# Kernel optimization log

Hardware: AMD Instinct MI355X
Metric: run time of the kernel (lower is better)

Reference implementation:

```python
import jax, jax.numpy as jnp
import numpy as np

HEADS = 4
DIM_HEAD = 64
DIM = 256
FMAP = 64
SCALE = DIM_HEAD ** -0.5


def setup_inputs() -> dict:
    key = jax.random.key(0)
    k1, k2, k3, k4 = jax.random.split(key, 4)
    inner = HEADS * DIM_HEAD
    fmap = jax.random.normal(k1, (4, DIM, FMAP, FMAP), dtype=jnp.float32)
    # 1x1 conv weight for qkv projection: (3*inner_dim, dim)
    w_qkv = jax.random.normal(k2, (3 * inner, DIM), dtype=jnp.float32) * (DIM ** -0.5)
    # AbsPosEmb parameters, initialized as randn * dim_head**-0.5 (as in BoTNet)
    pos_height = jax.random.normal(k3, (FMAP, DIM_HEAD), dtype=jnp.float32) * SCALE
    pos_width = jax.random.normal(k4, (FMAP, DIM_HEAD), dtype=jnp.float32) * SCALE
    return {"fmap": fmap, "w_qkv": w_qkv, "pos_height": pos_height, "pos_width": pos_width}


def reference(fmap, w_qkv, pos_height, pos_width):
    b, c, h, w = fmap.shape
    hw = h * w
    # 1x1 conv (no bias) == channel matmul
    qkv = jnp.einsum('bchw,oc->bohw', fmap, w_qkv)  # (b, 3*inner, h, w)
    q, k, v = jnp.split(qkv, 3, axis=1)
    # replicate torch .view(b, heads, h*w, -1): raw row-major reshape
    q = q.reshape(b, HEADS, hw, DIM_HEAD) * SCALE
    k = k.reshape(b, HEADS, hw, DIM_HEAD)
    v = v.reshape(b, HEADS, hw, DIM_HEAD)
    sim = jnp.einsum('bhid,bhjd->bhij', q, k)  # (b, heads, hw, hw)
    # absolute positional bias: emb[j] = height[y] + width[x], j = y*w + x
    emb = (pos_height[:, None, :] + pos_width[None, :, :]).reshape(hw, DIM_HEAD)
    sim = sim + jnp.einsum('bhid,jd->bhij', q, emb)
    attn = jax.nn.softmax(sim, axis=-1)
    out = jnp.einsum('bhij,bhjd->bhid', attn, v)  # (b, heads, hw, dim_head)
    # replicate torch .view(b, heads*dim_head, h, w): raw reshape
    return out.reshape(b, HEADS * DIM_HEAD, h, w)
```

## Files before the change

### kernel.cpp

```cpp
#include <hip/hip_runtime.h>


typedef float  f32x4  __attribute__((ext_vector_type(4)));
typedef __bf16 bf16x8 __attribute__((ext_vector_type(8)));
typedef __bf16 bf16x4 __attribute__((ext_vector_type(4)));

__device__ inline float fast_exp2(float x) {
#if __has_builtin(__builtin_amdgcn_exp2f)
  return __builtin_amdgcn_exp2f(x);
#else
  return exp2f(x);
#endif
}

__global__ __launch_bounds__(256) void qkv_proj(
    const float* __restrict__ fmap, const float* __restrict__ w,
    const float* __restrict__ ph,   const float* __restrict__ pw,
    __bf16* __restrict__ Qw, __bf16* __restrict__ Kw, __bf16* __restrict__ Vw)
{
  constexpr int LS = 136;
  __shared__ __bf16 As[64 * LS];
  __shared__ __bf16 Bs[64 * LS];
  const int tid  = threadIdx.x;
  const int wv   = tid >> 6;
  const int lane = tid & 63;
  const int quad = lane >> 4, l15 = lane & 15;
  const int n0 = blockIdx.x * 64;
  const int m0 = blockIdx.y * 64;
  const int b  = blockIdx.z;

  f32x4 sacc[4] = {};

  for (int ks = 0; ks < 2; ++ks) {
    const int kbase = ks * 128;
#pragma unroll
    for (int i = 0; i < 8; ++i) {
      int id = tid + i * 256;
      int r  = id >> 5;
      int c4 = (id & 31) * 4;
      f32x4 v = *(const f32x4*)(w + (size_t)(m0 + r) * 256 + kbase + c4);
      bf16x4 o; o[0]=(__bf16)v[0]; o[1]=(__bf16)v[1]; o[2]=(__bf16)v[2]; o[3]=(__bf16)v[3];
      *(bf16x4*)(&As[r * LS + c4]) = o;
    }
#pragma unroll
    for (int i = 0; i < 2; ++i) {
      int id = tid + i * 256;
      int sg = id & 15;
      int kg = id >> 4;
      const float* base = fmap + ((size_t)b * 256 + kbase + 4 * kg) * 4096 + n0 + 4 * sg;
      f32x4 v0 = *(const f32x4*)(base);
      f32x4 v1 = *(const f32x4*)(base + 4096);
      f32x4 v2 = *(const f32x4*)(base + 8192);
      f32x4 v3 = *(const f32x4*)(base + 12288);
#pragma unroll
      for (int j = 0; j < 4; ++j) {
        bf16x4 o; o[0]=(__bf16)v0[j]; o[1]=(__bf16)v1[j]; o[2]=(__bf16)v2[j]; o[3]=(__bf16)v3[j];
        *(bf16x4*)(&Bs[(4 * sg + j) * LS + 4 * kg]) = o;
      }
    }
    __syncthreads();
#pragma unroll
    for (int k0 = 0; k0 < 128; k0 += 32) {
      bf16x8 af = *(const bf16x8*)(&As[(16 * wv + l15) * LS + k0 + 8 * quad]);
#pragma unroll
      for (int t = 0; t < 4; ++t) {
        bf16x8 bt = *(const bf16x8*)(&Bs[(16 * t + l15) * LS + k0 + 8 * quad]);
        sacc[t] = __builtin_amdgcn_mfma_f32_16x16x32_bf16(af, bt, sacc[t], 0, 0, 0);
      }
    }
    __syncthreads();
  }

  const int region = blockIdx.y >> 2;
  const int obase  = (blockIdx.y & 3) * 64;
#pragma unroll
  for (int t = 0; t < 4; ++t) {
#pragma unroll
    for (int rr = 0; rr < 4; ++rr) {
      int row = 16 * wv + 4 * quad + rr;
      int s   = n0 + 16 * t + l15;
      float val = sacc[t][rr];
      size_t off = ((size_t)(b * 256 + obase + row)) * 4096 + s;
      if (region == 0) {
        Qw[off] = (__bf16)(val * 0.18033688f);
      } else if (region == 1) {
        float bias = ph[row * 64 + (s & 63)] + pw[(s >> 6) * 64 + (s & 63)];
        Kw[off] = (__bf16)(val + bias);
      } else {
        Vw[off] = (__bf16)val;
      }
    }
  }
}

__global__ __launch_bounds__(256) void v_transpose(
    const __bf16* __restrict__ Vw, __bf16* __restrict__ Vt)
{
  __shared__ __bf16 T[64 * 72];
  const int tid = threadIdx.x;
  const int j0  = blockIdx.x * 64;
  const int bh  = blockIdx.y;
  const __bf16* src = Vw + (size_t)bh * 262144;
#pragma unroll
  for (int i = 0; i < 2; ++i) {
    int id = tid + i * 256;
    int r = id >> 3, c = (id & 7) * 8;
    *(bf16x8*)(&T[r * 72 + c]) = *(const bf16x8*)(src + (size_t)(j0 + r) * 64 + c);
  }
  __syncthreads();
#pragma unroll
  for (int i = 0; i < 2; ++i) {
    int id = tid + i * 256;
    int d = id >> 3, jc = (id & 7) * 8;
    bf16x8 o;
#pragma unroll
    for (int z = 0; z < 8; ++z) o[z] = T[(jc + z) * 72 + d];
    *(bf16x8*)(Vt + ((size_t)bh * 64 + d) * 4096 + j0 + jc) = o;
  }
}

__global__ __launch_bounds__(256, 4) void flash_attn(
    const __bf16* __restrict__ Qg, const __bf16* __restrict__ Kg,
    const __bf16* __restrict__ Vtg, __bf16* __restrict__ OP0,
    float* __restrict__ lws, float* __restrict__ Og)
{
  __shared__ __bf16 Ks[64 * 64];
  __shared__ __bf16 Vs[64 * 64];
  const int tid  = threadIdx.x;
  const int wv   = tid >> 6;
  const int lane = tid & 63;
  const int quad = lane >> 4, l15 = lane & 15;
  const int bh = blockIdx.y;
  const int z  = blockIdx.z;
  const int iw = blockIdx.x * 128 + 32 * wv;
  const int jbase = z * 2048;
  const __bf16* Qb = Qg  + (size_t)bh * 262144;
  const __bf16* Kb = Kg  + (size_t)bh * 262144;
  const __bf16* Vb = Vtg + (size_t)bh * 262144;

  bf16x8 qf[2][2];
#pragma unroll
  for (int m = 0; m < 2; ++m)
#pragma unroll
    for (int c = 0; c < 2; ++c)
      qf[m][c] = *(const bf16x8*)(Qb + (size_t)(iw + 16 * m + l15) * 64 + 32 * c + 8 * quad);

  const int kr  = tid >> 3;
  const int kch = tid & 7;
  const int r0 = kr,      r1 = kr + 32;
  const int pr0 = (r0 & 0x23) | ((r0 & 0x0C) << 1) | ((r0 & 0x10) >> 2);
  const int pr1 = (r1 & 0x23) | ((r1 & 0x0C) << 1) | ((r1 & 0x10) >> 2);
  const int dst0 = r0 * 64 + ((kch ^ (r0 & 7)) * 8);
  const int dst1 = r1 * 64 + ((kch ^ (r1 & 7)) * 8);
  const __bf16* kp0 = Kb + (size_t)(jbase + pr0) * 64 + kch * 8;
  const __bf16* kp1 = Kb + (size_t)(jbase + pr1) * 64 + kch * 8;
  const __bf16* vp0 = Vb + (size_t)r0 * 4096 + jbase + kch * 8;
  const __bf16* vp1 = Vb + (size_t)r1 * 4096 + jbase + kch * 8;

  f32x4 acco[2][4] = {};
  f32x4 l4[2] = {};

  const int swz = (l15 & 7);

  for (int it = 0; it < 32; ++it) {
    bf16x8 k0 = *(const bf16x8*)kp0; kp0 += 4096;
    bf16x8 k1 = *(const bf16x8*)kp1; kp1 += 4096;
    bf16x8 v0 = *(const bf16x8*)vp0; vp0 += 64;
    bf16x8 v1 = *(const bf16x8*)vp1; vp1 += 64;
    *(bf16x8*)(&Ks[dst0]) = k0;
    *(bf16x8*)(&Ks[dst1]) = k1;
    *(bf16x8*)(&Vs[dst0]) = v0;
    *(bf16x8*)(&Vs[dst1]) = v1;
    __syncthreads();

    f32x4 sacc[2][4] = {};
#pragma unroll
    for (int c = 0; c < 2; ++c) {
#pragma unroll
      for (int t = 0; t < 4; ++t) {
        bf16x8 ak = *(const bf16x8*)(&Ks[(16 * t + l15) * 64 + (((4 * c + quad) ^ swz) * 8)]);
        sacc[0][t] = __builtin_amdgcn_mfma_f32_16x16x32_bf16(ak, qf[0][c], sacc[0][t], 0, 0, 0);
        sacc[1][t] = __builtin_amdgcn_mfma_f32_16x16x32_bf16(ak, qf[1][c], sacc[1][t], 0, 0, 0);
      }
    }

    bf16x8 pf[2][2];
#pragma unroll
    for (int m = 0; m < 2; ++m) {
#pragma unroll
      for (int t = 0; t < 4; ++t) {
#pragma unroll
        for (int r = 0; r < 4; ++r) {
          float pv = fast_exp2(sacc[m][t][r]);
          sacc[m][t][r] = pv;
          l4[m][r] += pv;
        }
      }
#pragma unroll
      for (int c2 = 0; c2 < 2; ++c2) {
        bf16x8 a;
#pragma unroll
        for (int r = 0; r < 4; ++r) {
          a[r]     = (__bf16)sacc[m][2 * c2][r];
          a[4 + r] = (__bf16)sacc[m][2 * c2 + 1][r];
        }
        pf[m][c2] = a;
      }
    }

#pragma unroll
    for (int c2 = 0; c2 < 2; ++c2) {
#pragma unroll
      for (int t = 0; t < 4; ++t) {
        bf16x8 bv = *(const bf16x8*)(&Vs[(16 * t + l15) * 64 + (((4 * c2 + quad) ^ swz) * 8)]);
        acco[0][t] = __builtin_amdgcn_mfma_f32_16x16x32_bf16(pf[0][c2], bv, acco[0][t], 0, 0, 0);
        acco[1][t] = __builtin_amdgcn_mfma_f32_16x16x32_bf16(pf[1][c2], bv, acco[1][t], 0, 0, 0);
      }
    }
    __syncthreads();
  }

#pragma unroll
  for (int m = 0; m < 2; ++m) {
    float l = (l4[m][0] + l4[m][1]) + (l4[m][2] + l4[m][3]);
    l += __shfl_xor(l, 16, 64);
    l += __shfl_xor(l, 32, 64);
    if (quad == 0)
      lws[z * 65536 + bh * 4096 + iw + 16 * m + l15] = l;
  }
  if (z == 0) {
    __bf16* Ob = OP0 + (size_t)bh * 262144;
#pragma unroll
    for (int m = 0; m < 2; ++m)
#pragma unroll
      for (int t = 0; t < 4; ++t)
#pragma unroll
        for (int r = 0; r < 4; ++r)
          Ob[(size_t)(iw + 16 * m + 4 * quad + r) * 64 + 16 * t + l15] =
              (__bf16)acco[m][t][r];
  } else {
    float* Ob = Og + (size_t)bh * 262144;
#pragma unroll
    for (int m = 0; m < 2; ++m)
#pragma unroll
      for (int t = 0; t < 4; ++t)
#pragma unroll
        for (int r = 0; r < 4; ++r)
          Ob[(size_t)(iw + 16 * m + 4 * quad + r) * 64 + 16 * t + l15] =
              acco[m][t][r];
  }
}

__global__ __launch_bounds__(256) void combine(
    const __bf16* __restrict__ OP0, const float* __restrict__ lws,
    float* __restrict__ Og)
{
  int idx = blockIdx.x * 256 + threadIdx.x;
  int row = idx >> 4;
  float inv = 1.0f / (lws[row] + lws[65536 + row]);
  f32x4 o = ((const f32x4*)Og)[idx];
  bf16x4 p = ((const bf16x4*)OP0)[idx];
  f32x4 r;
#pragma unroll
  for (int k = 0; k < 4; ++k) r[k] = (o[k] + (float)p[k]) * inv;
  ((f32x4*)Og)[idx] = r;
}

extern "C" void kernel_launch(void* const* d_in, const int* in_sizes, int n_in,
                              void* d_out, int out_size, void* d_ws, size_t ws_size,
                              hipStream_t stream) {
  const float* fmap = (const float*)d_in[0];
  const float* w    = (const float*)d_in[1];
  const float* ph   = (const float*)d_in[2];
  const float* pw   = (const float*)d_in[3];
  float* out = (float*)d_out;

  __bf16* Qw = (__bf16*)d_ws;
  __bf16* Kw = Qw + 4194304;
  __bf16* Vw = Kw + 4194304;
  __bf16* Vt = Vw + 4194304;
  float*  lws = (float*)(Vt + 4194304);

  qkv_proj   <<<dim3(64, 12, 4), 256, 0, stream>>>(fmap, w, ph, pw, Qw, Kw, Vw);
  v_transpose<<<dim3(64, 16),    256, 0, stream>>>(Vw, Vt);
  flash_attn <<<dim3(32, 16, 2), 256, 0, stream>>>(Qw, Kw, Vt, Vw , lws, out);
  combine    <<<dim3(4096),      256, 0, stream>>>(Vw , lws, out);
}
```

Baseline: 188.1 us.

## Pre-convert weights to bf16, stage fmap once per block, use direct LDS loads

A new small kernel converts the QKV weight to bf16 once per call. The projection kernel is restructured so each block loads a 32-column fmap tile into shared memory once and loops over all 12 output tiles, reading bf16 weights straight from global memory. Before, every output tile re-read and re-converted fmap. In flash attention, the K/V staging now uses global_load_lds to copy directly into LDS, with the XOR swizzle moved to the global source address instead of the LDS destination. The costs are an extra kernel launch, weight fragments read from global or cache inside the inner loop, and fewer, longer-running projection blocks.

```diff
diff --git a/kernel.cpp b/kernel.cpp
--- a/kernel.cpp
+++ b/kernel.cpp
@@ -13,81 +13,85 @@
 #endif
 }
 
+__device__ inline void glds16(const __bf16* g, __bf16* l) {
+  __builtin_amdgcn_global_load_lds(
+      (const __attribute__((address_space(1))) void*)g,
+      (__attribute__((address_space(3))) void*)l, 16, 0, 0);
+}
+
+__global__ __launch_bounds__(256) void w_cvt(
+    const float* __restrict__ w, __bf16* __restrict__ wb)
+{
+  int idx = blockIdx.x * 256 + threadIdx.x;
+  f32x4 v = ((const f32x4*)w)[idx];
+  bf16x4 o; o[0]=(__bf16)v[0]; o[1]=(__bf16)v[1]; o[2]=(__bf16)v[2]; o[3]=(__bf16)v[3];
+  ((bf16x4*)wb)[idx] = o;
+}
+
 __global__ __launch_bounds__(256) void qkv_proj(
-    const float* __restrict__ fmap, const float* __restrict__ w,
+    const float* __restrict__ fmap, const __bf16* __restrict__ wb,
     const float* __restrict__ ph,   const float* __restrict__ pw,
     __bf16* __restrict__ Qw, __bf16* __restrict__ Kw, __bf16* __restrict__ Vw)
 {
-  constexpr int LS = 136;
-  __shared__ __bf16 As[64 * LS];
-  __shared__ __bf16 Bs[64 * LS];
+  constexpr int LS = 264;
+  __shared__ __bf16 Bs[32 * LS];
   const int tid  = threadIdx.x;
   const int wv   = tid >> 6;
   const int lane = tid & 63;
   const int quad = lane >> 4, l15 = lane & 15;
-  const int n0 = blockIdx.x * 64;
-  const int m0 = blockIdx.y * 64;
-  const int b  = blockIdx.z;
-
-  f32x4 sacc[4] = {};
-
-  for (int ks = 0; ks < 2; ++ks) {
-    const int kbase = ks * 128;
-#pragma unroll
-    for (int i = 0; i < 8; ++i) {
-      int id = tid + i * 256;
-      int r  = id >> 5;
-      int c4 = (id & 31) * 4;
-      f32x4 v = *(const f32x4*)(w + (size_t)(m0 + r) * 256 + kbase + c4);
-      bf16x4 o; o[0]=(__bf16)v[0]; o[1]=(__bf16)v[1]; o[2]=(__bf16)v[2]; o[3]=(__bf16)v[3];
-      *(bf16x4*)(&As[r * LS + c4]) = o;
-    }
-#pragma unroll
-    for (int i = 0; i < 2; ++i) {
-      int id = tid + i * 256;
-      int sg = id & 15;
-      int kg = id >> 4;
-      const float* base = fmap + ((size_t)b * 256 + kbase + 4 * kg) * 4096 + n0 + 4 * sg;
-      f32x4 v0 = *(const f32x4*)(base);
-      f32x4 v1 = *(const f32x4*)(base + 4096);
-      f32x4 v2 = *(const f32x4*)(base + 8192);
-      f32x4 v3 = *(const f32x4*)(base + 12288);
-#pragma unroll
-      for (int j = 0; j < 4; ++j) {
-        bf16x4 o; o[0]=(__bf16)v0[j]; o[1]=(__bf16)v1[j]; o[2]=(__bf16)v2[j]; o[3]=(__bf16)v3[j];
-        *(bf16x4*)(&Bs[(4 * sg + j) * LS + 4 * kg]) = o;
-      }
-    }
-    __syncthreads();
-#pragma unroll
-    for (int k0 = 0; k0 < 128; k0 += 32) {
-      bf16x8 af = *(const bf16x8*)(&As[(16 * wv + l15) * LS + k0 + 8 * quad]);
-#pragma unroll
-      for (int t = 0; t < 4; ++t) {
-        bf16x8 bt = *(const bf16x8*)(&Bs[(16 * t + l15) * LS + k0 + 8 * quad]);
-        sacc[t] = __builtin_amdgcn_mfma_f32_16x16x32_bf16(af, bt, sacc[t], 0, 0, 0);
-      }
-    }
-    __syncthreads();
-  }
-
-  const int region = blockIdx.y >> 2;
-  const int obase  = (blockIdx.y & 3) * 64;
-#pragma unroll
-  for (int t = 0; t < 4; ++t) {
-#pragma unroll
-    for (int rr = 0; rr < 4; ++rr) {
-      int row = 16 * wv + 4 * quad + rr;
-      int s   = n0 + 16 * t + l15;
-      float val = sacc[t][rr];
-      size_t off = ((size_t)(b * 256 + obase + row)) * 4096 + s;
-      if (region == 0) {
-        Qw[off] = (__bf16)(val * 0.18033688f);
-      } else if (region == 1) {
-        float bias = ph[row * 64 + (s & 63)] + pw[(s >> 6) * 64 + (s & 63)];
-        Kw[off] = (__bf16)(val + bias);
-      } else {
-        Vw[off] = (__bf16)val;
+  const int n0 = blockIdx.x * 32;
+  const int b  = blockIdx.y;
+
+#pragma unroll
+  for (int i = 0; i < 2; ++i) {
+    int id = tid + i * 256;
+    int ng = id & 7;
+    int kg = id >> 3;
+    const float* base = fmap + ((size_t)b * 256 + 4 * kg) * 4096 + n0 + 4 * ng;
+    f32x4 v0 = *(const f32x4*)(base);
+    f32x4 v1 = *(const f32x4*)(base + 4096);
+    f32x4 v2 = *(const f32x4*)(base + 8192);
+    f32x4 v3 = *(const f32x4*)(base + 12288);
+#pragma unroll
+    for (int j = 0; j < 4; ++j) {
+      bf16x4 o; o[0]=(__bf16)v0[j]; o[1]=(__bf16)v1[j]; o[2]=(__bf16)v2[j]; o[3]=(__bf16)v3[j];
+      *(bf16x4*)(&Bs[(4 * ng + j) * LS + 4 * kg]) = o;
+    }
+  }
+  __syncthreads();
+
+  for (int mt = 0; mt < 12; ++mt) {
+    const int region = mt >> 2;
+    const int obase  = (mt & 3) * 64;
+    const __bf16* aptr = wb + (size_t)(mt * 64 + 16 * wv + l15) * 256 + 8 * quad;
+
+    f32x4 acc[2] = {};
+#pragma unroll
+    for (int k0 = 0; k0 < 256; k0 += 32) {
+      bf16x8 af = *(const bf16x8*)(aptr + k0);
+      bf16x8 b0 = *(const bf16x8*)(&Bs[(l15)      * LS + k0 + 8 * quad]);
+      bf16x8 b1 = *(const bf16x8*)(&Bs[(16 + l15) * LS + k0 + 8 * quad]);
+      acc[0] = __builtin_amdgcn_mfma_f32_16x16x32_bf16(af, b0, acc[0], 0, 0, 0);
+      acc[1] = __builtin_amdgcn_mfma_f32_16x16x32_bf16(af, b1, acc[1], 0, 0, 0);
+    }
+
+#pragma unroll
+    for (int t = 0; t < 2; ++t) {
+#pragma unroll
+      for (int rr = 0; rr < 4; ++rr) {
+        int oreg = obase + 16 * wv + 4 * quad + rr;
+        int s    = n0 + 16 * t + l15;
+        float val = acc[t][rr];
+        size_t off = ((size_t)(b * 256 + oreg)) * 4096 + s;
+        if (region == 0) {
+          Qw[off] = (__bf16)(val * 0.18033688f);
+        } else if (region == 1) {
+          int g = oreg & 63;
+          float bias = ph[g * 64 + (s & 63)] + pw[(s >> 6) * 64 + (s & 63)];
+          Kw[off] = (__bf16)(val + bias);
+        } else {
+          Vw[off] = (__bf16)val;
+        }
       }
     }
   }
@@ -145,17 +149,20 @@
     for (int c = 0; c < 2; ++c)
       qf[m][c] = *(const bf16x8*)(Qb + (size_t)(iw + 16 * m + l15) * 64 + 32 * c + 8 * quad);
 
-  const int kr  = tid >> 3;
+  const int r0  = tid >> 3;
   const int kch = tid & 7;
-  const int r0 = kr,      r1 = kr + 32;
-  const int pr0 = (r0 & 0x23) | ((r0 & 0x0C) << 1) | ((r0 & 0x10) >> 2);
-  const int pr1 = (r1 & 0x23) | ((r1 & 0x0C) << 1) | ((r1 & 0x10) >> 2);
-  const int dst0 = r0 * 64 + ((kch ^ (r0 & 7)) * 8);
-  const int dst1 = r1 * 64 + ((kch ^ (r1 & 7)) * 8);
-  const __bf16* kp0 = Kb + (size_t)(jbase + pr0) * 64 + kch * 8;
-  const __bf16* kp1 = Kb + (size_t)(jbase + pr1) * 64 + kch * 8;
-  const __bf16* vp0 = Vb + (size_t)r0 * 4096 + jbase + kch * 8;
-  const __bf16* vp1 = Vb + (size_t)r1 * 4096 + jbase + kch * 8;
+  const int xc  = (kch ^ (r0 & 7)) * 8;
+  const int pr0a = r0, pr1a = r0 + 32;
+  const int pr0 = (pr0a & 0x23) | ((pr0a & 0x0C) << 1) | ((pr0a & 0x10) >> 2);
+  const int pr1 = (pr1a & 0x23) | ((pr1a & 0x0C) << 1) | ((pr1a & 0x10) >> 2);
+  const __bf16* kp0 = Kb + (size_t)(jbase + pr0) * 64 + xc;
+  const __bf16* kp1 = Kb + (size_t)(jbase + pr1) * 64 + xc;
+  const __bf16* vp0 = Vb + (size_t)r0 * 4096        + jbase + xc;
+  const __bf16* vp1 = Vb + (size_t)(r0 + 32) * 4096 + jbase + xc;
+  __bf16* ldsK0 = &Ks[tid * 8];
+  __bf16* ldsK1 = &Ks[tid * 8 + 2048];
+  __bf16* ldsV0 = &Vs[tid * 8];
+  __bf16* ldsV1 = &Vs[tid * 8 + 2048];
 
   f32x4 acco[2][4] = {};
   f32x4 l4[2] = {};
@@ -163,14 +170,10 @@
   const int swz = (l15 & 7);
 
   for (int it = 0; it < 32; ++it) {
-    bf16x8 k0 = *(const bf16x8*)kp0; kp0 += 4096;
-    bf16x8 k1 = *(const bf16x8*)kp1; kp1 += 4096;
-    bf16x8 v0 = *(const bf16x8*)vp0; vp0 += 64;
-    bf16x8 v1 = *(const bf16x8*)vp1; vp1 += 64;
-    *(bf16x8*)(&Ks[dst0]) = k0;
-    *(bf16x8*)(&Ks[dst1]) = k1;
-    *(bf16x8*)(&Vs[dst0]) = v0;
-    *(bf16x8*)(&Vs[dst1]) = v1;
+    glds16(kp0, ldsK0); kp0 += 4096;
+    glds16(kp1, ldsK1); kp1 += 4096;
+    glds16(vp0, ldsV0); vp0 += 64;
+    glds16(vp1, ldsV1); vp1 += 64;
     __syncthreads();
 
     f32x4 sacc[2][4] = {};
@@ -280,8 +283,10 @@
   __bf16* Vw = Kw + 4194304;
   __bf16* Vt = Vw + 4194304;
   float*  lws = (float*)(Vt + 4194304);
-
-  qkv_proj   <<<dim3(64, 12, 4), 256, 0, stream>>>(fmap, w, ph, pw, Qw, Kw, Vw);
+  __bf16* Wb16 = (__bf16*)(lws + 131072);
+
+  w_cvt      <<<dim3(192),       256, 0, stream>>>(w, Wb16);
+  qkv_proj   <<<dim3(128, 4),    256, 0, stream>>>(fmap, Wb16, ph, pw, Qw, Kw, Vw);
   v_transpose<<<dim3(64, 16),    256, 0, stream>>>(Vw, Vt);
   flash_attn <<<dim3(32, 16, 2), 256, 0, stream>>>(Qw, Kw, Vt, Vw , lws, out);
   combine    <<<dim3(4096),      256, 0, stream>>>(Vw , lws, out);
```

Measured after the change: 185.9 us. Within noise of the previous version (-1.2%).
